# Performance work log

Hardware: AMD Instinct MI355X
Metric: run time of the kernel (lower is better)

Reference implementation:

```python
import jax, jax.numpy as jnp
import numpy as np

BETA = 0.25


def setup_inputs() -> dict:
    key = jax.random.key(0)
    k1, k2 = jax.random.split(key)
    inputs = jax.random.normal(k1, (32, 4096, 64), dtype=jnp.float32)
    # VarianceScaling(uniform) ~ small-magnitude init; plain normal scaled works for a numeric reference
    codebook = jax.random.normal(k2, (1024, 64), dtype=jnp.float32) * (1.0 / np.sqrt(64.0))
    return {"inputs": inputs, "codebook": codebook}


def reference(inputs, codebook):
    D = codebook.shape[-1]
    flat = jnp.reshape(inputs, (-1, D))                      # [N, D]
    flat_sqr = jnp.sum(flat ** 2, axis=-1, keepdims=True)    # [N, 1]
    code_sqr = jnp.sum(codebook ** 2, axis=-1)[None, :]      # [1, K]
    # full pairwise squared distances [N, K]
    distances = flat_sqr - 2.0 * (flat @ codebook.T) + code_sqr
    encoding_indices = jnp.reshape(jnp.argmin(distances, axis=-1), inputs.shape[:-1])
    quantize = codebook[encoding_indices]                    # gather -> [..., D]
    encoding_loss = jnp.mean((jax.lax.stop_gradient(inputs) - quantize) ** 2)
    commit_loss = jnp.mean((inputs - jax.lax.stop_gradient(quantize)) ** 2)
    loss = encoding_loss + BETA * commit_loss
    # straight-through estimator
    z_q = inputs + jax.lax.stop_gradient(quantize - inputs)
    return loss, z_q, encoding_indices
```

## Files before the change

### kernel.cpp

```cpp
#include <hip/hip_runtime.h>

#define N_ROWS 131072
#define D 64
#define K_CODES 1024

typedef _Float16 f16x8 __attribute__((ext_vector_type(8)));
typedef float    f32x4 __attribute__((ext_vector_type(4)));

#define MFMA16(a, b, c) __builtin_amdgcn_mfma_f32_16x16x32_f16((a), (b), (c), 0, 0, 0)

__global__ __launch_bounds__(256)
void prep_kernel(const float* __restrict__ CB, _Float16* __restrict__ CBf,
                 float* __restrict__ csqr, float* __restrict__ loss) {
    const int b = blockIdx.x, t = threadIdx.x;
    if (b < 64) {
        const int unit = b * 256 + t;
        const int tile = unit >> 8;
        const int f    = (unit >> 6) & 3;
        const int lane = unit & 63;
        const int quad = lane >> 4, lrow = lane & 15;
        const int code = tile * 16 + lrow;
        const int k0   = (f & 1) * 32 + quad * 8;
        const float* src = CB + (size_t)code * D + k0;
        float4 v0 = *(const float4*)(src);
        float4 v1 = *(const float4*)(src + 4);
        float xs[8] = {v0.x, v0.y, v0.z, v0.w, v1.x, v1.y, v1.z, v1.w};
        f16x8 o;
#pragma unroll
        for (int j = 0; j < 8; ++j) {
            _Float16 h = (_Float16)xs[j];
            o[j] = (f < 2) ? h : (_Float16)(xs[j] - (float)h);
        }
        *(f16x8*)(CBf + (size_t)unit * 8) = o;
    } else {
        if (t == 0) *loss = 0.0f;
        for (int k = t; k < K_CODES; k += 256) {
            const float4* p = (const float4*)(CB + (size_t)k * D);
            float s = 0.0f;
#pragma unroll
            for (int i = 0; i < 16; ++i) {
                float4 v = p[i];
                s += v.x * v.x + v.y * v.y + v.z * v.z + v.w * v.w;
            }
            csqr[k] = s;
        }
    }
}

__global__ __launch_bounds__(256, 4)
void argmin_kernel(const float* __restrict__ X,
                   const _Float16* __restrict__ CBf,
                   const float* __restrict__ csqr,
                   const float* __restrict__ CB,
                   float* __restrict__ out) {
    __shared__ float LsC[K_CODES];
    __shared__ float candD[64][2];
    __shared__ int   candI[64][2];
    __shared__ int   ivfin[64];
    __shared__ float xsqW[2];

    const int t    = threadIdx.x;
    const int wave = t >> 6;
    const int lane = t & 63;
    const int lrow = lane & 15;
    const int quad = lane >> 4;
    const int rh   = wave >> 1;
    const int ch   = wave & 1;
    const int R0   = blockIdx.x * 64;
    const int Rw   = R0 + rh * 32;

    ((float4*)LsC)[t] = ((const float4*)csqr)[t];

    f16x8 Ah[2][2], Al[2][2];
    float xsq = 0.0f;
#pragma unroll
    for (int mt = 0; mt < 2; ++mt) {
        const float* xr = X + (size_t)(Rw + mt * 16 + lrow) * D;
#pragma unroll
        for (int ks = 0; ks < 2; ++ks) {
            const int k0 = ks * 32 + quad * 8;
            float4 v0 = *(const float4*)(xr + k0);
            float4 v1 = *(const float4*)(xr + k0 + 4);
            float xs[8] = {v0.x, v0.y, v0.z, v0.w, v1.x, v1.y, v1.z, v1.w};
            f16x8 h, l;
#pragma unroll
            for (int j = 0; j < 8; ++j) {
                xsq += xs[j] * xs[j];
                float sv = -2.0f * xs[j];
                _Float16 hh = (_Float16)sv;
                h[j] = hh;
                l[j] = (_Float16)(sv - (float)hh);
            }
            Ah[mt][ks] = h;
            Al[mt][ks] = l;
        }
    }
    __syncthreads();

    float bestd[2][4];
    int   besti[2][4];
#pragma unroll
    for (int mt = 0; mt < 2; ++mt)
#pragma unroll
        for (int r = 0; r < 4; ++r) { bestd[mt][r] = 3.0e38f; besti[mt][r] = 0; }

    const f16x8* gw = (const f16x8*)CBf + (size_t)ch * 32 * 256 + lane;

#define LOADB(Bv, tl)                                                         \
    do {                                                                      \
        const f16x8* _p = gw + (tl) * 256;                                    \
        Bv[0] = _p[0]; Bv[1] = _p[64]; Bv[2] = _p[128]; Bv[3] = _p[192];      \
    } while (0)

#define COMPUTE(Bv, tl)                                                       \
    do {                                                                      \
        const int   c  = (ch * 32 + (tl)) * 16 + lrow;                        \
        const float cs = LsC[c];                                              \
        _Pragma("unroll")                                                     \
        for (int mt = 0; mt < 2; ++mt) {                                      \
            f32x4 acc = {cs, cs, cs, cs};                                     \
            acc = MFMA16(Ah[mt][0], Bv[0], acc);                              \
            acc = MFMA16(Ah[mt][1], Bv[1], acc);                              \
            acc = MFMA16(Al[mt][0], Bv[0], acc);                              \
            acc = MFMA16(Al[mt][1], Bv[1], acc);                              \
            acc = MFMA16(Ah[mt][0], Bv[2], acc);                              \
            acc = MFMA16(Ah[mt][1], Bv[3], acc);                              \
            _Pragma("unroll")                                                 \
            for (int r = 0; r < 4; ++r) {                                     \
                bool lt = acc[r] < bestd[mt][r];                              \
                bestd[mt][r] = lt ? acc[r] : bestd[mt][r];                    \
                besti[mt][r] = lt ? c : besti[mt][r];                         \
            }                                                                 \
        }                                                                     \
    } while (0)

    f16x8 Ba[4], Bb[4];
    LOADB(Ba, 0);
    for (int tl = 0; tl < 32; tl += 2) {
        LOADB(Bb, tl + 1);
        COMPUTE(Ba, tl);
        LOADB(Ba, tl + 2);
        COMPUTE(Bb, tl + 1);
    }

    if (ch == 0) {
        float s = xsq;
#pragma unroll
        for (int m = 1; m < 64; m <<= 1) s += __shfl_xor(s, m, 64);
        if (lane == 0) xsqW[rh] = s;
    }

#pragma unroll
    for (int mt = 0; mt < 2; ++mt) {
#pragma unroll
        for (int r = 0; r < 4; ++r) {
            float dv = bestd[mt][r];
            int   iv = besti[mt][r];
#pragma unroll
            for (int m = 1; m < 16; m <<= 1) {
                float od = __shfl_xor(dv, m, 64);
                int   oi = __shfl_xor(iv, m, 64);
                if (od < dv || (od == dv && oi < iv)) { dv = od; iv = oi; }
            }
            if (lrow == 0) {
                int rl = rh * 32 + mt * 16 + quad * 4 + r;
                candD[rl][ch] = dv;
                candI[rl][ch] = iv;
            }
        }
    }
    __syncthreads();

    const float scale = 1.25f / (float)((size_t)N_ROWS * D);
    if (t < 64) {
        float d0 = candD[t][0], d1 = candD[t][1];
        int   i0 = candI[t][0], i1 = candI[t][1];
        bool take1 = d1 < d0;
        float dv = take1 ? d1 : d0;
        int   iv = take1 ? i1 : i0;
        out[1 + (size_t)N_ROWS * D + R0 + t] = (float)iv;
        ivfin[t] = iv;
        float ssum = dv;
#pragma unroll
        for (int m = 1; m < 64; m <<= 1) ssum += __shfl_xor(ssum, m, 64);
        if (t == 0)
            atomicAdd(out, (ssum + xsqW[0] + xsqW[1]) * scale);
    }
    __syncthreads();

    float* p = out + 1 + (size_t)R0 * D;
#pragma unroll
    for (int i = 0; i < 4; ++i) {
        int q = i * 256 + t;
        int j = 4 * q + 3;
        if (q < 1023) {
            float v[4];
#pragma unroll
            for (int e = 0; e < 4; ++e) {
                int jj = j + e;
                v[e] = CB[(size_t)ivfin[jj >> 6] * D + (jj & 63)];
            }
            *(float4*)(p + j) = make_float4(v[0], v[1], v[2], v[3]);
        } else if (q == 1023) {
            p[4095] = CB[(size_t)ivfin[63] * D + 63];
        }
    }
    if (t == 0) {
        const float* c0 = CB + (size_t)ivfin[0] * D;
        p[0] = c0[0];
        p[1] = c0[1];
        p[2] = c0[2];
    }
}

extern "C" void kernel_launch(void* const* d_in, const int* in_sizes, int n_in,
                              void* d_out, int out_size, void* d_ws,
                              size_t ws_size, hipStream_t stream) {
    const float* X  = (const float*)d_in[0];
    const float* CB = (const float*)d_in[1];

    float*    csqr = (float*)d_ws;
    _Float16* CBf  = (_Float16*)((char*)d_ws + 4096);

    hipLaunchKernelGGL(prep_kernel, dim3(65), dim3(256), 0, stream,
                       CB, CBf, csqr, (float*)d_out);
    hipLaunchKernelGGL(argmin_kernel, dim3(N_ROWS / 64), dim3(256), 0, stream,
                       X, CBf, csqr, CB, (float*)d_out);
}
```

Baseline: 170.7 us.

## Give each wave all 64 rows and a quarter of the codebook

```diff
diff --git a/kernel.cpp b/kernel.cpp
--- a/kernel.cpp
+++ b/kernel.cpp
@@ -47,35 +47,32 @@
     }
 }
 
-__global__ __launch_bounds__(256, 4)
+__global__ __launch_bounds__(256, 3)
 void argmin_kernel(const float* __restrict__ X,
                    const _Float16* __restrict__ CBf,
                    const float* __restrict__ csqr,
                    const float* __restrict__ CB,
                    float* __restrict__ out) {
     __shared__ float LsC[K_CODES];
-    __shared__ float candD[64][2];
-    __shared__ int   candI[64][2];
+    __shared__ float candD[64][4];
+    __shared__ int   candI[64][4];
     __shared__ int   ivfin[64];
-    __shared__ float xsqW[2];
+    __shared__ float xsqS;
 
     const int t    = threadIdx.x;
-    const int wave = t >> 6;
+    const int cq   = t >> 6;
     const int lane = t & 63;
     const int lrow = lane & 15;
     const int quad = lane >> 4;
-    const int rh   = wave >> 1;
-    const int ch   = wave & 1;
     const int R0   = blockIdx.x * 64;
-    const int Rw   = R0 + rh * 32;
 
     ((float4*)LsC)[t] = ((const float4*)csqr)[t];
 
-    f16x8 Ah[2][2], Al[2][2];
+    f16x8 Ah[4][2], Al[4][2];
     float xsq = 0.0f;
 #pragma unroll
-    for (int mt = 0; mt < 2; ++mt) {
-        const float* xr = X + (size_t)(Rw + mt * 16 + lrow) * D;
+    for (int mt = 0; mt < 4; ++mt) {
+        const float* xr = X + (size_t)(R0 + mt * 16 + lrow) * D;
 #pragma unroll
         for (int ks = 0; ks < 2; ++ks) {
             const int k0 = ks * 32 + quad * 8;
@@ -97,14 +94,14 @@
     }
     __syncthreads();
 
-    float bestd[2][4];
-    int   besti[2][4];
-#pragma unroll
-    for (int mt = 0; mt < 2; ++mt)
+    float bestd[4][4];
+    int   besti[4][4];
+#pragma unroll
+    for (int mt = 0; mt < 4; ++mt)
 #pragma unroll
         for (int r = 0; r < 4; ++r) { bestd[mt][r] = 3.0e38f; besti[mt][r] = 0; }
 
-    const f16x8* gw = (const f16x8*)CBf + (size_t)ch * 32 * 256 + lane;
+    const f16x8* gw = (const f16x8*)CBf + (size_t)cq * 16 * 256 + lane;
 
 #define LOADB(Bv, tl)                                                         \
     do {                                                                      \
@@ -114,10 +111,10 @@
 
 #define COMPUTE(Bv, tl)                                                       \
     do {                                                                      \
-        const int   c  = (ch * 32 + (tl)) * 16 + lrow;                        \
+        const int   c  = (cq * 16 + (tl)) * 16 + lrow;                        \
         const float cs = LsC[c];                                              \
         _Pragma("unroll")                                                     \
-        for (int mt = 0; mt < 2; ++mt) {                                      \
+        for (int mt = 0; mt < 4; ++mt) {                                      \
             f32x4 acc = {cs, cs, cs, cs};                                     \
             acc = MFMA16(Ah[mt][0], Bv[0], acc);                              \
             acc = MFMA16(Ah[mt][1], Bv[1], acc);                              \
@@ -134,24 +131,32 @@
         }                                                                     \
     } while (0)
 
-    f16x8 Ba[4], Bb[4];
-    LOADB(Ba, 0);
-    for (int tl = 0; tl < 32; tl += 2) {
-        LOADB(Bb, tl + 1);
-        COMPUTE(Ba, tl);
-        LOADB(Ba, tl + 2);
-        COMPUTE(Bb, tl + 1);
-    }
-
-    if (ch == 0) {
+    f16x8 B0[4], B1[4], B2[4];
+    LOADB(B0, 0);
+    LOADB(B1, 1);
+#pragma unroll
+    for (int tl = 0; tl < 16; tl += 3) {
+        LOADB(B2, tl + 2);
+        COMPUTE(B0, tl);
+        if (tl + 1 < 16) {
+            LOADB(B0, tl + 3);
+            COMPUTE(B1, tl + 1);
+        }
+        if (tl + 2 < 16) {
+            LOADB(B1, tl + 4);
+            COMPUTE(B2, tl + 2);
+        }
+    }
+
+    if (cq == 0) {
         float s = xsq;
 #pragma unroll
         for (int m = 1; m < 64; m <<= 1) s += __shfl_xor(s, m, 64);
-        if (lane == 0) xsqW[rh] = s;
-    }
-
-#pragma unroll
-    for (int mt = 0; mt < 2; ++mt) {
+        if (lane == 0) xsqS = s;
+    }
+
+#pragma unroll
+    for (int mt = 0; mt < 4; ++mt) {
 #pragma unroll
         for (int r = 0; r < 4; ++r) {
             float dv = bestd[mt][r];
@@ -163,9 +168,9 @@
                 if (od < dv || (od == dv && oi < iv)) { dv = od; iv = oi; }
             }
             if (lrow == 0) {
-                int rl = rh * 32 + mt * 16 + quad * 4 + r;
-                candD[rl][ch] = dv;
-                candI[rl][ch] = iv;
+                int rl = mt * 16 + quad * 4 + r;
+                candD[rl][cq] = dv;
+                candI[rl][cq] = iv;
             }
         }
     }
@@ -173,18 +178,21 @@
 
     const float scale = 1.25f / (float)((size_t)N_ROWS * D);
     if (t < 64) {
-        float d0 = candD[t][0], d1 = candD[t][1];
-        int   i0 = candI[t][0], i1 = candI[t][1];
-        bool take1 = d1 < d0;
-        float dv = take1 ? d1 : d0;
-        int   iv = take1 ? i1 : i0;
+        float dv = candD[t][0];
+        int   iv = candI[t][0];
+#pragma unroll
+        for (int q = 1; q < 4; ++q) {
+            float dq = candD[t][q];
+            int   iq = candI[t][q];
+            if (dq < dv) { dv = dq; iv = iq; }
+        }
         out[1 + (size_t)N_ROWS * D + R0 + t] = (float)iv;
         ivfin[t] = iv;
         float ssum = dv;
 #pragma unroll
         for (int m = 1; m < 64; m <<= 1) ssum += __shfl_xor(ssum, m, 64);
         if (t == 0)
-            atomicAdd(out, (ssum + xsqW[0] + xsqW[1]) * scale);
+            atomicAdd(out, (ssum + xsqS) * scale);
     }
     __syncthreads();
 
```

Result: slower. 391.6 us (+129.4%).

## Stage codebook chunks into LDS with async copies and give each wave 32 rows

Applied to the files above, without the earlier changes.

```diff
diff --git a/kernel.cpp b/kernel.cpp
--- a/kernel.cpp
+++ b/kernel.cpp
@@ -3,11 +3,19 @@
 #define N_ROWS 131072
 #define D 64
 #define K_CODES 1024
+#define RPB 128
+#define CH_TILES 4
+#define NCHUNK 16
 
 typedef _Float16 f16x8 __attribute__((ext_vector_type(8)));
 typedef float    f32x4 __attribute__((ext_vector_type(4)));
 
 #define MFMA16(a, b, c) __builtin_amdgcn_mfma_f32_16x16x32_f16((a), (b), (c), 0, 0, 0)
+
+#define ASYNC_COPY16(gp, lp)                                                  \
+    __builtin_amdgcn_global_load_lds(                                         \
+        (const __attribute__((address_space(1))) void*)(gp),                  \
+        (__attribute__((address_space(3))) void*)(lp), 16, 0, 0)
 
 __global__ __launch_bounds__(256)
 void prep_kernel(const float* __restrict__ CB, _Float16* __restrict__ CBf,
@@ -53,21 +61,17 @@
                    const float* __restrict__ csqr,
                    const float* __restrict__ CB,
                    float* __restrict__ out) {
+    __shared__ __align__(16) _Float16 Bs[2][CH_TILES * 256 * 8];
     __shared__ float LsC[K_CODES];
-    __shared__ float candD[64][2];
-    __shared__ int   candI[64][2];
-    __shared__ int   ivfin[64];
-    __shared__ float xsqW[2];
+    __shared__ int   ivfin[RPB];
 
     const int t    = threadIdx.x;
     const int wave = t >> 6;
     const int lane = t & 63;
     const int lrow = lane & 15;
     const int quad = lane >> 4;
-    const int rh   = wave >> 1;
-    const int ch   = wave & 1;
-    const int R0   = blockIdx.x * 64;
-    const int Rw   = R0 + rh * 32;
+    const int R0   = blockIdx.x * RPB;
+    const int Rw   = R0 + wave * 32;
 
     ((float4*)LsC)[t] = ((const float4*)csqr)[t];
 
@@ -95,7 +99,6 @@
             Al[mt][ks] = l;
         }
     }
-    __syncthreads();
 
     float bestd[2][4];
     int   besti[2][4];
@@ -104,52 +107,53 @@
 #pragma unroll
         for (int r = 0; r < 4; ++r) { bestd[mt][r] = 3.0e38f; besti[mt][r] = 0; }
 
-    const f16x8* gw = (const f16x8*)CBf + (size_t)ch * 32 * 256 + lane;
-
-#define LOADB(Bv, tl)                                                         \
+#define STAGE(c, b)                                                           \
     do {                                                                      \
-        const f16x8* _p = gw + (tl) * 256;                                    \
-        Bv[0] = _p[0]; Bv[1] = _p[64]; Bv[2] = _p[128]; Bv[3] = _p[192];      \
+        const char* gb = (const char*)CBf + (size_t)(c) * 16384               \
+                         + wave * 4096 + lane * 16;                           \
+        _Float16* lb = &Bs[b][wave * 2048];             \
+        ASYNC_COPY16(gb,        lb);                                          \
+        ASYNC_COPY16(gb + 1024, lb + 512);                                    \
+        ASYNC_COPY16(gb + 2048, lb + 1024);                                   \
+        ASYNC_COPY16(gb + 3072, lb + 1536);                                   \
     } while (0)
 
-#define COMPUTE(Bv, tl)                                                       \
-    do {                                                                      \
-        const int   c  = (ch * 32 + (tl)) * 16 + lrow;                        \
-        const float cs = LsC[c];                                              \
-        _Pragma("unroll")                                                     \
-        for (int mt = 0; mt < 2; ++mt) {                                      \
-            f32x4 acc = {cs, cs, cs, cs};                                     \
-            acc = MFMA16(Ah[mt][0], Bv[0], acc);                              \
-            acc = MFMA16(Ah[mt][1], Bv[1], acc);                              \
-            acc = MFMA16(Al[mt][0], Bv[0], acc);                              \
-            acc = MFMA16(Al[mt][1], Bv[1], acc);                              \
-            acc = MFMA16(Ah[mt][0], Bv[2], acc);                              \
-            acc = MFMA16(Ah[mt][1], Bv[3], acc);                              \
-            _Pragma("unroll")                                                 \
-            for (int r = 0; r < 4; ++r) {                                     \
-                bool lt = acc[r] < bestd[mt][r];                              \
-                bestd[mt][r] = lt ? acc[r] : bestd[mt][r];                    \
-                besti[mt][r] = lt ? c : besti[mt][r];                         \
-            }                                                                 \
-        }                                                                     \
-    } while (0)
-
-    f16x8 Ba[4], Bb[4];
-    LOADB(Ba, 0);
-    for (int tl = 0; tl < 32; tl += 2) {
-        LOADB(Bb, tl + 1);
-        COMPUTE(Ba, tl);
-        LOADB(Ba, tl + 2);
-        COMPUTE(Bb, tl + 1);
-    }
-
-    if (ch == 0) {
-        float s = xsq;
-#pragma unroll
-        for (int m = 1; m < 64; m <<= 1) s += __shfl_xor(s, m, 64);
-        if (lane == 0) xsqW[rh] = s;
-    }
-
+    STAGE(0, 0);
+    __syncthreads();
+
+    for (int c = 0; c < NCHUNK; ++c) {
+        const int cb = c & 1;
+        if (c + 1 < NCHUNK) STAGE(c + 1, (c + 1) & 1);
+
+#pragma unroll
+        for (int tl = 0; tl < CH_TILES; ++tl) {
+            const f16x8* bu = (const f16x8*)&Bs[cb][0] + tl * 256 + lane;
+            f16x8 Bh0 = bu[0], Bh1 = bu[64], Bl0 = bu[128], Bl1 = bu[192];
+            const int   cc = (c * CH_TILES + tl) * 16 + lrow;
+            const float cs = LsC[cc];
+#pragma unroll
+            for (int mt = 0; mt < 2; ++mt) {
+                f32x4 acc = {cs, cs, cs, cs};
+                acc = MFMA16(Ah[mt][0], Bh0, acc);
+                acc = MFMA16(Ah[mt][1], Bh1, acc);
+                acc = MFMA16(Al[mt][0], Bh0, acc);
+                acc = MFMA16(Al[mt][1], Bh1, acc);
+                acc = MFMA16(Ah[mt][0], Bl0, acc);
+                acc = MFMA16(Ah[mt][1], Bl1, acc);
+#pragma unroll
+                for (int r = 0; r < 4; ++r) {
+                    bool lt = acc[r] < bestd[mt][r];
+                    bestd[mt][r] = lt ? acc[r] : bestd[mt][r];
+                    besti[mt][r] = lt ? cc : besti[mt][r];
+                }
+            }
+        }
+        __syncthreads();
+    }
+
+    const float scale = 1.25f / (float)((size_t)N_ROWS * D);
+
+    float ssum = 0.0f;
 #pragma unroll
     for (int mt = 0; mt < 2; ++mt) {
 #pragma unroll
@@ -163,37 +167,26 @@
                 if (od < dv || (od == dv && oi < iv)) { dv = od; iv = oi; }
             }
             if (lrow == 0) {
-                int rl = rh * 32 + mt * 16 + quad * 4 + r;
-                candD[rl][ch] = dv;
-                candI[rl][ch] = iv;
-            }
-        }
-    }
+                int rl = wave * 32 + mt * 16 + quad * 4 + r;
+                ivfin[rl] = iv;
+                out[1 + (size_t)N_ROWS * D + R0 + rl] = (float)iv;
+                ssum += dv;
+            }
+        }
+    }
+    ssum += __shfl_xor(ssum, 16, 64);
+    ssum += __shfl_xor(ssum, 32, 64);
+#pragma unroll
+    for (int m = 1; m < 64; m <<= 1) xsq += __shfl_xor(xsq, m, 64);
+    if (lane == 0) atomicAdd(out, (ssum + xsq) * scale);
     __syncthreads();
 
-    const float scale = 1.25f / (float)((size_t)N_ROWS * D);
-    if (t < 64) {
-        float d0 = candD[t][0], d1 = candD[t][1];
-        int   i0 = candI[t][0], i1 = candI[t][1];
-        bool take1 = d1 < d0;
-        float dv = take1 ? d1 : d0;
-        int   iv = take1 ? i1 : i0;
-        out[1 + (size_t)N_ROWS * D + R0 + t] = (float)iv;
-        ivfin[t] = iv;
-        float ssum = dv;
-#pragma unroll
-        for (int m = 1; m < 64; m <<= 1) ssum += __shfl_xor(ssum, m, 64);
-        if (t == 0)
-            atomicAdd(out, (ssum + xsqW[0] + xsqW[1]) * scale);
-    }
-    __syncthreads();
-
     float* p = out + 1 + (size_t)R0 * D;
 #pragma unroll
-    for (int i = 0; i < 4; ++i) {
+    for (int i = 0; i < 8; ++i) {
         int q = i * 256 + t;
         int j = 4 * q + 3;
-        if (q < 1023) {
+        if (q < 2047) {
             float v[4];
 #pragma unroll
             for (int e = 0; e < 4; ++e) {
@@ -201,8 +194,8 @@
                 v[e] = CB[(size_t)ivfin[jj >> 6] * D + (jj & 63)];
             }
             *(float4*)(p + j) = make_float4(v[0], v[1], v[2], v[3]);
-        } else if (q == 1023) {
-            p[4095] = CB[(size_t)ivfin[63] * D + 63];
+        } else if (q == 2047) {
+            p[8191] = CB[(size_t)ivfin[RPB - 1] * D + 63];
         }
     }
     if (t == 0) {
@@ -224,6 +217,6 @@
 
     hipLaunchKernelGGL(prep_kernel, dim3(65), dim3(256), 0, stream,
                        CB, CBf, csqr, (float*)d_out);
-    hipLaunchKernelGGL(argmin_kernel, dim3(N_ROWS / 64), dim3(256), 0, stream,
+    hipLaunchKernelGGL(argmin_kernel, dim3(N_ROWS / RPB), dim3(256), 0, stream,
                        X, CBf, csqr, CB, (float*)d_out);
 }
```

After: 176.9 us. 3.7% more time.
